# Optimization experiments

Hardware: AMD Instinct MI355X
Metric: run time of the kernel (lower is better)

Reference implementation:

```python
import jax, jax.numpy as jnp
import numpy as np

N, K, F, H, C = 16384, 16, 3, 64, 10


def setup_inputs() -> dict:
    key = jax.random.key(0)
    ks = jax.random.split(key, 6)
    pos = jax.random.normal(ks[0], (N, F), jnp.float32)
    batch = jnp.zeros((N,), jnp.int32)  # single graph
    W1 = jax.random.normal(ks[1], (2 * F, H), jnp.float32) * 0.1
    b1 = jnp.zeros((H,), jnp.float32)
    W2 = jax.random.normal(ks[2], (2 * H, H), jnp.float32) * 0.1
    b2 = jnp.zeros((H,), jnp.float32)
    Wc = jax.random.normal(ks[3], (H, C), jnp.float32) * 0.1
    bc = jnp.zeros((C,), jnp.float32)
    return {"pos": pos, "batch": batch, "W1": W1, "b1": b1,
            "W2": W2, "b2": b2, "Wc": Wc, "bc": bc}


def knn_graph(pos, k):
    # brute-force knn with self-loops (loop=True): self has distance 0
    sq = jnp.sum(pos * pos, axis=1)
    d = sq[:, None] + sq[None, :] - 2.0 * (pos @ pos.T)  # [N, N]
    _, idx = jax.lax.top_k(-d, k)  # [N, k] nearest neighbor indices (incl. self)
    return idx


def edge_conv(x, idx, W, b):
    # message for edge j->i: Linear(concat(x_i, x_j - x_i)); aggregate by max over neighbors
    n, k = idx.shape
    xi = x[:, None, :]               # [N, 1, F]
    xj = x[idx]                      # [N, k, F]
    msg = jnp.concatenate([jnp.broadcast_to(xi, (n, k, x.shape[1])), xj - xi], axis=-1)
    m = msg @ W + b                  # [N, k, H]
    return jnp.max(m, axis=1)        # [N, H]


def reference(pos, batch, W1, b1, W2, b2, Wc, bc):
    idx = knn_graph(pos, K)
    h = jax.nn.relu(edge_conv(pos, idx, W1, b1))
    h = jax.nn.relu(edge_conv(h, idx, W2, b2))
    g = jax.ops.segment_max(h, batch, num_segments=1)  # global max pool -> [1, H]
    return g @ Wc + bc
```

## Files before the change

### kernel.cpp

```cpp
#include <hip/hip_runtime.h>

#define NPTS 16384
#define KNN 16
#define HID 64
#define NCLS 10

#define CHUNKS_T 16
#define CHUNK_T (NPTS / CHUNKS_T)
#define NSTR 16
#define SCAP 128

__device__ __forceinline__ float distf(float4 q, float4 p) {
    float dot = fmaf(q.x, p.x, fmaf(q.y, p.y, q.z * p.z));
    return fmaf(-2.f, dot, p.w);
}

__device__ __forceinline__ unsigned long long dkey(float v, int j) {
    unsigned u = __float_as_uint(v);
    u = (u & 0x80000000u) ? ~u : (u | 0x80000000u);
    return ((unsigned long long)u << 32) | (unsigned)j;
}

__device__ __forceinline__ unsigned long long shfl_xor_u64(unsigned long long x, int m) {
    unsigned hi = (unsigned)__shfl_xor((int)(x >> 32), m, 64);
    unsigned lo = (unsigned)__shfl_xor((int)(x & 0xffffffffu), m, 64);
    return ((unsigned long long)hi << 32) | lo;
}

__device__ __forceinline__ void wave_top16_16(unsigned long long (&key)[16], int lane,
                                              int q, int* __restrict__ idx) {
    int outj = 0x7fffffff;
    for (int r = 0; r < 16; ++r) {
        unsigned long long gm = key[0];
#pragma unroll
        for (int s = 1; s < 16; ++s) gm = key[s] < gm ? key[s] : gm;
#pragma unroll
        for (int st = 1; st < 64; st <<= 1) {
            unsigned long long o = shfl_xor_u64(gm, st);
            gm = o < gm ? o : gm;
        }
        if (lane == r) outj = (int)(gm & 0xffffffffu);
#pragma unroll
        for (int s = 0; s < 16; ++s)
            if (key[s] == gm) key[s] = ~0ull;
    }
    if (lane < 16) idx[q * KNN + lane] = outj;
}

__global__ void prep_kernel(const float* __restrict__ pos, float4* __restrict__ pos4) {
    int i = blockIdx.x * 256 + threadIdx.x;
    if (i < NPTS) {
        float x = pos[3 * i], y = pos[3 * i + 1], z = pos[3 * i + 2];
        pos4[i] = make_float4(x, y, z, fmaf(x, x, fmaf(y, y, z * z)));
    }
}

__global__ __launch_bounds__(256) void knn_tau_kernel(const float4* __restrict__ pos4,
                                                      float* __restrict__ minpart) {
    int tid = threadIdx.x;
    int q0 = blockIdx.x * 512 + tid;
    int q1 = q0 + 256;
    int c = blockIdx.y;
    float4 qa = pos4[q0];
    float4 qb = pos4[q1];
    float mna[NSTR], mnb[NSTR];
#pragma unroll
    for (int u = 0; u < NSTR; ++u) { mna[u] = INFINITY; mnb[u] = INFINITY; }
    __shared__ float4 tile[256];
    int base = c * CHUNK_T;
    for (int t0 = 0; t0 < CHUNK_T; t0 += 256) {
        __syncthreads();
        tile[tid] = pos4[base + t0 + tid];
        __syncthreads();
        for (int jj = 0; jj < 256; jj += NSTR) {
#pragma unroll
            for (int u = 0; u < NSTR; ++u) {
                float4 p = tile[jj + u];
                mna[u] = fminf(mna[u], distf(qa, p));
                mnb[u] = fminf(mnb[u], distf(qb, p));
            }
        }
    }
#pragma unroll
    for (int u = 0; u < NSTR; ++u) {
        minpart[(c * NSTR + u) * NPTS + q0] = mna[u];
        minpart[(c * NSTR + u) * NPTS + q1] = mnb[u];
    }
}

__global__ __launch_bounds__(256) void knn_tau_reduce_kernel(const float* __restrict__ minpart,
                                                             float* __restrict__ tau) {
    int q = blockIdx.x * 256 + threadIdx.x;
    float t = -INFINITY;
#pragma unroll
    for (int u = 0; u < NSTR; ++u) {
        float m = INFINITY;
#pragma unroll
        for (int c = 0; c < CHUNKS_T; ++c) m = fminf(m, minpart[(c * NSTR + u) * NPTS + q]);
        t = fmaxf(t, m);
    }
    tau[q] = t;
}

__global__ __launch_bounds__(256) void knn_fused_kernel(const float4* __restrict__ pos4,
                                                        const float* __restrict__ tau,
                                                        int* __restrict__ idx) {
    __shared__ float4 tile[256];
    __shared__ unsigned long long keys[16][SCAP];
    __shared__ int knt[16];
    int tid = threadIdx.x;
    int lane = tid & 63;
    int w = tid >> 6;
    int qb = blockIdx.x * 16 + w * 4;
    float4 qp0 = pos4[qb + 0], qp1 = pos4[qb + 1], qp2 = pos4[qb + 2], qp3 = pos4[qb + 3];
    float tq0 = tau[qb + 0], tq1 = tau[qb + 1], tq2 = tau[qb + 2], tq3 = tau[qb + 3];
    if (lane < 4) knt[w * 4 + lane] = 0;
    for (int tb = 0; tb < NPTS; tb += 256) {
        __syncthreads();
        tile[tid] = pos4[tb + tid];
        __syncthreads();
#pragma unroll
        for (int r = 0; r < 4; ++r) {
            int jj = r * 64 + lane;
            float4 p = tile[jj];
            int j = tb + jj;
            float v0 = distf(qp0, p);
            float v1 = distf(qp1, p);
            float v2 = distf(qp2, p);
            float v3 = distf(qp3, p);
            if (v0 <= tq0) { int s = atomicAdd(&knt[w * 4 + 0], 1); if (s < SCAP) keys[w * 4 + 0][s] = dkey(v0, j); }
            if (v1 <= tq1) { int s = atomicAdd(&knt[w * 4 + 1], 1); if (s < SCAP) keys[w * 4 + 1][s] = dkey(v1, j); }
            if (v2 <= tq2) { int s = atomicAdd(&knt[w * 4 + 2], 1); if (s < SCAP) keys[w * 4 + 2][s] = dkey(v2, j); }
            if (v3 <= tq3) { int s = atomicAdd(&knt[w * 4 + 3], 1); if (s < SCAP) keys[w * 4 + 3][s] = dkey(v3, j); }
        }
    }
#pragma unroll
    for (int qi = 0; qi < 4; ++qi) {
        int q = qb + qi;
        int ntot = knt[w * 4 + qi];
        if (ntot <= SCAP) {
            unsigned long long k0 = (lane < ntot) ? keys[w * 4 + qi][lane] : ~0ull;
            unsigned long long k1 = (lane + 64 < ntot) ? keys[w * 4 + qi][lane + 64] : ~0ull;
            int r0 = 0, r1 = 0;
            for (int t = 0; t < ntot; ++t) {
                unsigned long long k = keys[w * 4 + qi][t];
                r0 += (int)(k < k0);
                r1 += (int)(k < k1);
            }
            if (lane < ntot && r0 < KNN) idx[q * KNN + r0] = (int)(k0 & 0xffffffffu);
            if (lane + 64 < ntot && r1 < KNN) idx[q * KNN + r1] = (int)(k1 & 0xffffffffu);
        } else {
            float tq = tau[q];
            float4 qq = pos4[q];
            unsigned long long key[16];
#pragma unroll
            for (int u = 0; u < 16; ++u) key[u] = ~0ull;
            for (int j = lane; j < NPTS; j += 64) {
                float v = distf(qq, pos4[j]);
                unsigned long long k = dkey(v, j);
                if (v <= tq && k < key[15]) {
#pragma unroll
                    for (int s = 0; s < 16; ++s) {
                        unsigned long long mn = k < key[s] ? k : key[s];
                        unsigned long long mx = k < key[s] ? key[s] : k;
                        key[s] = mn;
                        k = mx;
                    }
                }
            }
            wave_top16_16(key, lane, q, idx);
        }
    }
}


__global__ __launch_bounds__(256) void ec1_pre_kernel(const float4* __restrict__ pos4,
                                                      const float* __restrict__ W1,
                                                      const float* __restrict__ b1,
                                                      float* __restrict__ C1,
                                                      float* __restrict__ Y1) {
    int t = threadIdx.x & 63;
    int p = blockIdx.x * 4 + (threadIdx.x >> 6);
    float4 x = pos4[p];
    float w0 = W1[0 * HID + t], w1 = W1[1 * HID + t], w2 = W1[2 * HID + t];
    float v0 = W1[3 * HID + t], v1 = W1[4 * HID + t], v2 = W1[5 * HID + t];
    float y = fmaf(x.x, v0, fmaf(x.y, v1, x.z * v2));
    float cc = b1[t] + x.x * (w0 - v0) + x.y * (w1 - v1) + x.z * (w2 - v2);
    Y1[p * HID + t] = y;
    C1[p * HID + t] = cc;
}

__global__ __launch_bounds__(256) void ec1_max_kernel(const float* __restrict__ C1,
                                                      const float* __restrict__ Y1,
                                                      const int* __restrict__ idx,
                                                      float* __restrict__ h1) {
    int t = threadIdx.x & 63;
    int p = blockIdx.x * 4 + (threadIdx.x >> 6);
    float m = -INFINITY;
#pragma unroll
    for (int k = 0; k < KNN; ++k) {
        int j = idx[p * KNN + k];
        m = fmaxf(m, Y1[j * HID + t]);
    }
    h1[p * HID + t] = fmaxf(C1[p * HID + t] + m, 0.f);
}

__global__ __launch_bounds__(256) void ec2_pre_kernel(const float* __restrict__ h1,
                                                      const float* __restrict__ W2,
                                                      const float* __restrict__ b2,
                                                      float* __restrict__ C2,
                                                      float* __restrict__ Y2) {
    int t = threadIdx.x & 63;
    int r = threadIdx.x >> 6;
    int pb = blockIdx.x * 16 + r * 4;
    float aa[4] = {0.f, 0.f, 0.f, 0.f};
    float ab[4] = {0.f, 0.f, 0.f, 0.f};
#pragma unroll 8
    for (int f = 0; f < 64; ++f) {
        float wa = W2[f * HID + t];
        float wb = W2[(64 + f) * HID + t];
#pragma unroll
        for (int i = 0; i < 4; ++i) {
            float h = h1[(pb + i) * HID + f];
            aa[i] = fmaf(h, wa, aa[i]);
            ab[i] = fmaf(h, wb, ab[i]);
        }
    }
    float bt = b2[t];
#pragma unroll
    for (int i = 0; i < 4; ++i) {
        C2[(pb + i) * HID + t] = bt + aa[i] - ab[i];
        Y2[(pb + i) * HID + t] = ab[i];
    }
}

__global__ __launch_bounds__(256) void ec2_maxpool_kernel(const float* __restrict__ C2,
                                                          const float* __restrict__ Y2,
                                                          const int* __restrict__ idx,
                                                          float* __restrict__ gpartial) {
    int t = threadIdx.x & 63;
    int lp = threadIdx.x >> 6;
    int p = blockIdx.x * 4 + lp;
    float m = -INFINITY;
#pragma unroll
    for (int k = 0; k < KNN; ++k) {
        int j = idx[p * KNN + k];
        m = fmaxf(m, Y2[j * HID + t]);
    }
    float val = fmaxf(C2[p * HID + t] + m, 0.f);
    __shared__ float red[4][64];
    red[lp][t] = val;
    __syncthreads();
    if (lp == 0) {
        float g = fmaxf(fmaxf(red[0][t], red[1][t]), fmaxf(red[2][t], red[3][t]));
        gpartial[blockIdx.x * 64 + t] = g;
    }
}

__global__ __launch_bounds__(256) void greduce2_kernel(const float* __restrict__ gpartial,
                                                       float* __restrict__ gp2) {
    __shared__ float red[4][64];
    int f = threadIdx.x & 63;
    int w = threadIdx.x >> 6;
    int r0 = blockIdx.x * 16 + w * 4;
    float m = -INFINITY;
#pragma unroll
    for (int r = 0; r < 4; ++r) m = fmaxf(m, gpartial[(r0 + r) * 64 + f]);
    red[w][f] = m;
    __syncthreads();
    if (w == 0)
        gp2[blockIdx.x * 64 + f] =
            fmaxf(fmaxf(red[0][f], red[1][f]), fmaxf(red[2][f], red[3][f]));
}

__global__ __launch_bounds__(256) void tail2_kernel(const float* __restrict__ gp2,
                                                    const float* __restrict__ Wc,
                                                    const float* __restrict__ bc,
                                                    float* __restrict__ out) {
    __shared__ float red[4][64];
    __shared__ float g[64];
    int f = threadIdx.x & 63;
    int w = threadIdx.x >> 6;
    float m = -INFINITY;
    for (int i = w; i < 256; i += 4) m = fmaxf(m, gp2[i * 64 + f]);
    red[w][f] = m;
    __syncthreads();
    if (w == 0) g[f] = fmaxf(fmaxf(red[0][f], red[1][f]), fmaxf(red[2][f], red[3][f]));
    __syncthreads();
    if (threadIdx.x < NCLS) {
        float a = bc[threadIdx.x];
#pragma unroll
        for (int h = 0; h < HID; ++h) a = fmaf(g[h], Wc[h * NCLS + threadIdx.x], a);
        out[threadIdx.x] = a;
    }
}

extern "C" void kernel_launch(void* const* d_in, const int* in_sizes, int n_in,
                              void* d_out, int out_size, void* d_ws, size_t ws_size,
                              hipStream_t stream) {
    const float* pos = (const float*)d_in[0];
    const float* W1 = (const float*)d_in[2];
    const float* b1 = (const float*)d_in[3];
    const float* W2 = (const float*)d_in[4];
    const float* b2 = (const float*)d_in[5];
    const float* Wc = (const float*)d_in[6];
    const float* bc = (const float*)d_in[7];
    float* out = (float*)d_out;

    char* ws = (char*)d_ws;
    size_t o = 0;
    auto alloc = [&](size_t bytes) { size_t r = o; o += (bytes + 255) & ~size_t(255); return r; };
    size_t sz_minp = (size_t)NPTS * CHUNKS_T * NSTR * 4;
    size_t sz_cy = (size_t)NPTS * HID * 4 * 4;
    size_t o_pos4 = alloc((size_t)NPTS * 16);
    size_t o_shared = alloc(sz_minp > sz_cy ? sz_minp : sz_cy);
    size_t o_tau = alloc((size_t)NPTS * 4);
    size_t o_idx = alloc((size_t)NPTS * KNN * 4);
    size_t o_h1 = alloc((size_t)NPTS * HID * 4);
    size_t o_gp = alloc((size_t)(NPTS / 4) * HID * 4);
    size_t o_gp2 = alloc((size_t)256 * HID * 4);

    float4* pos4 = (float4*)(ws + o_pos4);
    float* minp = (float*)(ws + o_shared);
    size_t fm = (size_t)NPTS * HID * 4;
    float* C1 = (float*)(ws + o_shared + 0 * fm);
    float* Y1 = (float*)(ws + o_shared + 1 * fm);
    float* C2 = (float*)(ws + o_shared + 2 * fm);
    float* Y2 = (float*)(ws + o_shared + 3 * fm);
    float* tau = (float*)(ws + o_tau);
    int* idx = (int*)(ws + o_idx);
    float* h1 = (float*)(ws + o_h1);
    float* gp = (float*)(ws + o_gp);
    float* gp2 = (float*)(ws + o_gp2);

    prep_kernel<<<NPTS / 256, 256, 0, stream>>>(pos, pos4);
    knn_tau_kernel<<<dim3(NPTS / 512, CHUNKS_T), 256, 0, stream>>>(pos4, minp);
    knn_tau_reduce_kernel<<<NPTS / 256, 256, 0, stream>>>(minp, tau);
    knn_fused_kernel<<<NPTS / 16, 256, 0, stream>>>(pos4, tau, idx);
    ec1_pre_kernel<<<NPTS / 4, 256, 0, stream>>>(pos4, W1, b1, C1, Y1);
    ec1_max_kernel<<<NPTS / 4, 256, 0, stream>>>(C1, Y1, idx, h1);
    ec2_pre_kernel<<<NPTS / 16, 256, 0, stream>>>(h1, W2, b2, C2, Y2);
    ec2_maxpool_kernel<<<NPTS / 4, 256, 0, stream>>>(C2, Y2, idx, gp);
    greduce2_kernel<<<256, 256, 0, stream>>>(gp, gp2);
    tail2_kernel<<<1, 256, 0, stream>>>(gp2, Wc, bc, out);
}
```

Before: 342.7 us.

## Fuse kNN threshold computation into the candidate-selection kernel via wave shuffles

Drops the separate tau-partial and tau-reduce kernels and the minpart buffer. The single knn kernel now makes two passes over all points per wave of 2 queries. The first pass computes per-lane minima and reduces them with shuffles: min across lanes 16 and 32 apart, then max over the 16 groups. This gives a threshold that keeps at least 16 candidates; the second pass collects those candidates as before. The aim is to cut two launches and the partial-minima global traffic. In exchange, each query pair re-reads every point twice and fewer queries share each LDS tile, so distance and memory work per query rises.

```diff
diff --git a/kernel.cpp b/kernel.cpp
--- a/kernel.cpp
+++ b/kernel.cpp
@@ -5,9 +5,8 @@
 #define HID 64
 #define NCLS 10
 
-#define CHUNKS_T 16
-#define CHUNK_T (NPTS / CHUNKS_T)
-#define NSTR 16
+#define QPB 8
+#define QPW 2
 #define SCAP 128
 
 __device__ __forceinline__ float distf(float4 q, float4 p) {
@@ -55,102 +54,74 @@
     }
 }
 
-__global__ __launch_bounds__(256) void knn_tau_kernel(const float4* __restrict__ pos4,
-                                                      float* __restrict__ minpart) {
-    int tid = threadIdx.x;
-    int q0 = blockIdx.x * 512 + tid;
-    int q1 = q0 + 256;
-    int c = blockIdx.y;
-    float4 qa = pos4[q0];
-    float4 qb = pos4[q1];
-    float mna[NSTR], mnb[NSTR];
-#pragma unroll
-    for (int u = 0; u < NSTR; ++u) { mna[u] = INFINITY; mnb[u] = INFINITY; }
+__global__ __launch_bounds__(256) void knn_kernel(const float4* __restrict__ pos4,
+                                                  int* __restrict__ idx) {
     __shared__ float4 tile[256];
-    int base = c * CHUNK_T;
-    for (int t0 = 0; t0 < CHUNK_T; t0 += 256) {
-        __syncthreads();
-        tile[tid] = pos4[base + t0 + tid];
-        __syncthreads();
-        for (int jj = 0; jj < 256; jj += NSTR) {
-#pragma unroll
-            for (int u = 0; u < NSTR; ++u) {
-                float4 p = tile[jj + u];
-                mna[u] = fminf(mna[u], distf(qa, p));
-                mnb[u] = fminf(mnb[u], distf(qb, p));
-            }
-        }
-    }
-#pragma unroll
-    for (int u = 0; u < NSTR; ++u) {
-        minpart[(c * NSTR + u) * NPTS + q0] = mna[u];
-        minpart[(c * NSTR + u) * NPTS + q1] = mnb[u];
-    }
-}
-
-__global__ __launch_bounds__(256) void knn_tau_reduce_kernel(const float* __restrict__ minpart,
-                                                             float* __restrict__ tau) {
-    int q = blockIdx.x * 256 + threadIdx.x;
-    float t = -INFINITY;
-#pragma unroll
-    for (int u = 0; u < NSTR; ++u) {
-        float m = INFINITY;
-#pragma unroll
-        for (int c = 0; c < CHUNKS_T; ++c) m = fminf(m, minpart[(c * NSTR + u) * NPTS + q]);
-        t = fmaxf(t, m);
-    }
-    tau[q] = t;
-}
-
-__global__ __launch_bounds__(256) void knn_fused_kernel(const float4* __restrict__ pos4,
-                                                        const float* __restrict__ tau,
-                                                        int* __restrict__ idx) {
-    __shared__ float4 tile[256];
-    __shared__ unsigned long long keys[16][SCAP];
-    __shared__ int knt[16];
+    __shared__ unsigned long long keys[QPB][SCAP];
+    __shared__ int knt[QPB];
     int tid = threadIdx.x;
     int lane = tid & 63;
     int w = tid >> 6;
-    int qb = blockIdx.x * 16 + w * 4;
-    float4 qp0 = pos4[qb + 0], qp1 = pos4[qb + 1], qp2 = pos4[qb + 2], qp3 = pos4[qb + 3];
-    float tq0 = tau[qb + 0], tq1 = tau[qb + 1], tq2 = tau[qb + 2], tq3 = tau[qb + 3];
-    if (lane < 4) knt[w * 4 + lane] = 0;
+    int qb = blockIdx.x * QPB + w * QPW;
+    float4 q0 = pos4[qb + 0], q1 = pos4[qb + 1];
+
+    float m0 = INFINITY, m1 = INFINITY;
     for (int tb = 0; tb < NPTS; tb += 256) {
         __syncthreads();
         tile[tid] = pos4[tb + tid];
         __syncthreads();
 #pragma unroll
         for (int r = 0; r < 4; ++r) {
+            float4 p = tile[r * 64 + lane];
+            m0 = fminf(m0, distf(q0, p));
+            m1 = fminf(m1, distf(q1, p));
+        }
+    }
+    m0 = fminf(m0, __shfl_xor(m0, 16, 64));
+    m1 = fminf(m1, __shfl_xor(m1, 16, 64));
+    m0 = fminf(m0, __shfl_xor(m0, 32, 64));
+    m1 = fminf(m1, __shfl_xor(m1, 32, 64));
+#pragma unroll
+    for (int mk = 1; mk <= 8; mk <<= 1) {
+        m0 = fmaxf(m0, __shfl_xor(m0, mk, 64));
+        m1 = fmaxf(m1, __shfl_xor(m1, mk, 64));
+    }
+    float tq0 = m0, tq1 = m1;
+    if (lane < QPW) knt[w * QPW + lane] = 0;
+
+    for (int tb = 0; tb < NPTS; tb += 256) {
+        __syncthreads();
+        tile[tid] = pos4[tb + tid];
+        __syncthreads();
+#pragma unroll
+        for (int r = 0; r < 4; ++r) {
             int jj = r * 64 + lane;
             float4 p = tile[jj];
             int j = tb + jj;
-            float v0 = distf(qp0, p);
-            float v1 = distf(qp1, p);
-            float v2 = distf(qp2, p);
-            float v3 = distf(qp3, p);
-            if (v0 <= tq0) { int s = atomicAdd(&knt[w * 4 + 0], 1); if (s < SCAP) keys[w * 4 + 0][s] = dkey(v0, j); }
-            if (v1 <= tq1) { int s = atomicAdd(&knt[w * 4 + 1], 1); if (s < SCAP) keys[w * 4 + 1][s] = dkey(v1, j); }
-            if (v2 <= tq2) { int s = atomicAdd(&knt[w * 4 + 2], 1); if (s < SCAP) keys[w * 4 + 2][s] = dkey(v2, j); }
-            if (v3 <= tq3) { int s = atomicAdd(&knt[w * 4 + 3], 1); if (s < SCAP) keys[w * 4 + 3][s] = dkey(v3, j); }
-        }
-    }
-#pragma unroll
-    for (int qi = 0; qi < 4; ++qi) {
+            float v0 = distf(q0, p);
+            float v1 = distf(q1, p);
+            if (v0 <= tq0) { int s = atomicAdd(&knt[w * QPW + 0], 1); if (s < SCAP) keys[w * QPW + 0][s] = dkey(v0, j); }
+            if (v1 <= tq1) { int s = atomicAdd(&knt[w * QPW + 1], 1); if (s < SCAP) keys[w * QPW + 1][s] = dkey(v1, j); }
+        }
+    }
+
+#pragma unroll
+    for (int qi = 0; qi < QPW; ++qi) {
         int q = qb + qi;
-        int ntot = knt[w * 4 + qi];
+        int ntot = knt[w * QPW + qi];
         if (ntot <= SCAP) {
-            unsigned long long k0 = (lane < ntot) ? keys[w * 4 + qi][lane] : ~0ull;
-            unsigned long long k1 = (lane + 64 < ntot) ? keys[w * 4 + qi][lane + 64] : ~0ull;
+            unsigned long long k0 = (lane < ntot) ? keys[w * QPW + qi][lane] : ~0ull;
+            unsigned long long k1 = (lane + 64 < ntot) ? keys[w * QPW + qi][lane + 64] : ~0ull;
             int r0 = 0, r1 = 0;
             for (int t = 0; t < ntot; ++t) {
-                unsigned long long k = keys[w * 4 + qi][t];
+                unsigned long long k = keys[w * QPW + qi][t];
                 r0 += (int)(k < k0);
                 r1 += (int)(k < k1);
             }
             if (lane < ntot && r0 < KNN) idx[q * KNN + r0] = (int)(k0 & 0xffffffffu);
             if (lane + 64 < ntot && r1 < KNN) idx[q * KNN + r1] = (int)(k1 & 0xffffffffu);
         } else {
-            float tq = tau[q];
+            float tq = (qi == 0) ? tq0 : tq1;
             float4 qq = pos4[q];
             unsigned long long key[16];
 #pragma unroll
@@ -310,33 +281,29 @@
     char* ws = (char*)d_ws;
     size_t o = 0;
     auto alloc = [&](size_t bytes) { size_t r = o; o += (bytes + 255) & ~size_t(255); return r; };
-    size_t sz_minp = (size_t)NPTS * CHUNKS_T * NSTR * 4;
-    size_t sz_cy = (size_t)NPTS * HID * 4 * 4;
+    size_t fm = (size_t)NPTS * HID * 4;
     size_t o_pos4 = alloc((size_t)NPTS * 16);
-    size_t o_shared = alloc(sz_minp > sz_cy ? sz_minp : sz_cy);
-    size_t o_tau = alloc((size_t)NPTS * 4);
     size_t o_idx = alloc((size_t)NPTS * KNN * 4);
-    size_t o_h1 = alloc((size_t)NPTS * HID * 4);
+    size_t o_h1 = alloc(fm);
+    size_t o_C1 = alloc(fm);
+    size_t o_Y1 = alloc(fm);
+    size_t o_C2 = alloc(fm);
+    size_t o_Y2 = alloc(fm);
     size_t o_gp = alloc((size_t)(NPTS / 4) * HID * 4);
     size_t o_gp2 = alloc((size_t)256 * HID * 4);
 
     float4* pos4 = (float4*)(ws + o_pos4);
-    float* minp = (float*)(ws + o_shared);
-    size_t fm = (size_t)NPTS * HID * 4;
-    float* C1 = (float*)(ws + o_shared + 0 * fm);
-    float* Y1 = (float*)(ws + o_shared + 1 * fm);
-    float* C2 = (float*)(ws + o_shared + 2 * fm);
-    float* Y2 = (float*)(ws + o_shared + 3 * fm);
-    float* tau = (float*)(ws + o_tau);
     int* idx = (int*)(ws + o_idx);
     float* h1 = (float*)(ws + o_h1);
+    float* C1 = (float*)(ws + o_C1);
+    float* Y1 = (float*)(ws + o_Y1);
+    float* C2 = (float*)(ws + o_C2);
+    float* Y2 = (float*)(ws + o_Y2);
     float* gp = (float*)(ws + o_gp);
     float* gp2 = (float*)(ws + o_gp2);
 
     prep_kernel<<<NPTS / 256, 256, 0, stream>>>(pos, pos4);
-    knn_tau_kernel<<<dim3(NPTS / 512, CHUNKS_T), 256, 0, stream>>>(pos4, minp);
-    knn_tau_reduce_kernel<<<NPTS / 256, 256, 0, stream>>>(minp, tau);
-    knn_fused_kernel<<<NPTS / 16, 256, 0, stream>>>(pos4, tau, idx);
+    knn_kernel<<<NPTS / QPB, 256, 0, stream>>>(pos4, idx);
     ec1_pre_kernel<<<NPTS / 4, 256, 0, stream>>>(pos4, W1, b1, C1, Y1);
     ec1_max_kernel<<<NPTS / 4, 256, 0, stream>>>(C1, Y1, idx, h1);
     ec2_pre_kernel<<<NPTS / 16, 256, 0, stream>>>(h1, W2, b2, C2, Y2);
```

New measurement: 362.5 us. 5.8% more time.
